# Kernel tuning notes

Hardware: AMD Instinct MI355X
Metric: run time of the kernel (lower is better)

## Reference

```python
import jax, jax.numpy as jnp
import numpy as np

B, N, D, H, DK, DV = 2, 2048, 1024, 16, 64, 64
NEG = -1000000000.0
EPS = 1e-6


def setup_inputs() -> dict:
    key = jax.random.key(0)
    ks = jax.random.split(key, 8)
    s = 0.02
    return {
        "q": jax.random.normal(ks[0], (B, N, D), jnp.float32),
        "k": jax.random.normal(ks[1], (B, N, D), jnp.float32),
        "v": jax.random.normal(ks[2], (B, N, D), jnp.float32),
        "attn_mask": jnp.ones((B, N, N), jnp.int32),
        "Wq": jax.random.normal(ks[3], (D, H * DK), jnp.float32) * s,
        "Wk": jax.random.normal(ks[4], (D, H * DK), jnp.float32) * s,
        "Wv": jax.random.normal(ks[5], (D, H * DV), jnp.float32) * s,
        "Wo": jax.random.normal(ks[6], (H * DV, D), jnp.float32) * s,
        "gamma": jnp.ones((D,), jnp.float32),
        "beta": jnp.zeros((D,), jnp.float32),
    }


def reference(q, k, v, attn_mask, Wq, Wk, Wv, Wo, gamma, beta):
    b, n, _ = q.shape
    residual = q
    # project and split heads: (b, h, n, dk)
    qh = (q @ Wq).reshape(b, n, H, DK).transpose(0, 2, 1, 3)
    kh = (k @ Wk).reshape(b, n, H, DK).transpose(0, 2, 1, 3)
    vh = (v @ Wv).reshape(b, n, H, DV).transpose(0, 2, 1, 3)
    temperature = DK ** 0.5
    scores = jnp.einsum('bhnd,bhmd->bhnm', qh / temperature, kh)
    # external mask (masked where mask == 0), broadcast over heads
    scores = jnp.where(attn_mask[:, None, :, :] == 0, NEG, scores)
    # built-in causal mask (strictly upper triangle)
    causal = jnp.triu(jnp.ones((n, n), dtype=bool), k=1)
    scores = jnp.where(causal, NEG, scores)
    attn = jax.nn.softmax(scores, axis=-1)
    out = jnp.einsum('bhnm,bhmd->bnhd', attn, vh).reshape(b, n, H * DV)
    out = out @ Wo + residual
    # LayerNorm(eps=1e-6)
    mean = out.mean(-1, keepdims=True)
    var = ((out - mean) ** 2).mean(-1, keepdims=True)
    out = (out - mean) / jnp.sqrt(var + EPS) * gamma + beta
    return out, attn
```

## Files before the change

kernel.cpp:

```cpp
#include <hip/hip_runtime.h>
#include <hip/hip_bf16.h>
#include <stdint.h>

#define B_ 2
#define N_ 2048
#define D_ 1024
#define H_ 16
#define MM 4096
#define NN 1024
#define KK 1024

typedef __bf16 bf16;
typedef __bf16 bf16x8 __attribute__((ext_vector_type(8)));
typedef float f32x4 __attribute__((ext_vector_type(4)));

struct __align__(8) bf4 { bf16 v[4]; };

#define LDS_STRIDE 144
#define PSTR 272
#define LOG2E 1.44269504088896340736f

__global__ __launch_bounds__(256) void k_prep(const float* __restrict__ Wq,
                                              const float* __restrict__ Wk,
                                              const float* __restrict__ Wv,
                                              const float* __restrict__ Wo,
                                              const int* __restrict__ mask,
                                              bf16* __restrict__ WqT,
                                              bf16* __restrict__ WkT,
                                              bf16* __restrict__ WvT,
                                              bf16* __restrict__ WoT,
                                              uint32_t* __restrict__ bits) {
    __shared__ float tl[32][33];
    const int bid = blockIdx.x;
    if (bid < 4096) {
        const int z = bid >> 10, t = bid & 1023;
        const float* W = z == 0 ? Wq : z == 1 ? Wk : z == 2 ? Wv : Wo;
        bf16* Wt = z == 0 ? WqT : z == 1 ? WkT : z == 2 ? WvT : WoT;
        const int bx = (t & 31) * 32, by = (t >> 5) * 32;
        const int tx = threadIdx.x & 31, ty = threadIdx.x >> 5;
#pragma unroll
        for (int j = 0; j < 32; j += 8)
            tl[ty + j][tx] = W[(size_t)(by + ty + j) * 1024 + bx + tx];
        __syncthreads();
#pragma unroll
        for (int j = 0; j < 32; j += 8)
            Wt[(size_t)(bx + ty + j) * 1024 + by + tx] = (bf16)tl[tx][ty + j];
    } else {
        size_t flat = (size_t)(bid - 4096) * 256 + threadIdx.x;
        int col = (int)(flat & (N_ - 1));
        int row = (int)((flat >> 11) & (N_ - 1));
        bool ok = (mask[flat] != 0) && (col <= row);
        unsigned long long bal = __ballot(ok);
        if ((threadIdx.x & 63) == 0)
            *(unsigned long long*)(bits + (flat >> 5)) = bal;
    }
}

template <bool AF32>
__device__ __forceinline__ void kb_core(const void* __restrict__ Av,
                                        const bf16* __restrict__ Bt,
                                        int bm0, int bn0,
                                        char* AsB, char* BsB,
                                        f32x4 (&acc)[4][2]) {
    const int tid = threadIdx.x, lane = tid & 63, w = tid >> 6;
    const int g = lane >> 4, li = lane & 15;
    const int srow = tid >> 3, sc = tid & 7;
    const bf16* Ab = (const bf16*)Av;
    const float* Af = (const float*)Av;

    f32x4 zz = {0.f, 0.f, 0.f, 0.f};
#pragma unroll
    for (int mf = 0; mf < 4; ++mf)
#pragma unroll
        for (int nf = 0; nf < 2; ++nf) acc[mf][nf] = zz;

    f32x4 pa0[2], pa1[2];
    bf16x8 pab[2];
    bf16x8 pb[4];

    auto issueA = [&](int k0) {
        if constexpr (AF32) {
#pragma unroll
            for (int i = 0; i < 2; ++i) {
                const float* s = Af + (size_t)(bm0 + srow + 32 * i) * KK + k0 + sc * 8;
                pa0[i] = *(const f32x4*)s;
                pa1[i] = *(const f32x4*)(s + 4);
            }
        } else {
#pragma unroll
            for (int i = 0; i < 2; ++i)
                pab[i] = *(const bf16x8*)(Ab + (size_t)(bm0 + srow + 32 * i) * KK + k0 + sc * 8);
        }
    };
    auto issueB = [&](int k0) {
#pragma unroll
        for (int i = 0; i < 4; ++i)
            pb[i] = *(const bf16x8*)(Bt + (size_t)(bn0 + srow + 32 * i) * KK + k0 + sc * 8);
    };
    auto writeS = [&]() {
#pragma unroll
        for (int i = 0; i < 2; ++i) {
            bf16x8 t;
            if constexpr (AF32) {
#pragma unroll
                for (int j = 0; j < 4; ++j) {
                    t[j] = (bf16)pa0[i][j];
                    t[4 + j] = (bf16)pa1[i][j];
                }
            } else {
                t = pab[i];
            }
            *(bf16x8*)(AsB + (srow + 32 * i) * LDS_STRIDE + sc * 16) = t;
        }
#pragma unroll
        for (int i = 0; i < 4; ++i)
            *(bf16x8*)(BsB + (srow + 32 * i) * LDS_STRIDE + sc * 16) = pb[i];
    };

    issueA(0);
    issueB(0);
    for (int k0 = 0; k0 < KK; k0 += 64) {
        __syncthreads();
        writeS();
        int kn = (k0 + 64 < KK) ? k0 + 64 : k0;
        issueA(kn);
        issueB(kn);
        __syncthreads();
#pragma unroll
        for (int kk = 0; kk < 2; ++kk) {
            const int kb = kk * 64 + (g << 4);
            bf16x8 bfr[2];
#pragma unroll
            for (int nf = 0; nf < 2; ++nf) {
                int rn = w * 32 + nf * 16 + li;
                bfr[nf] = *(const bf16x8*)(BsB + rn * LDS_STRIDE + kb);
            }
#pragma unroll
            for (int mf = 0; mf < 4; ++mf) {
                int rm = mf * 16 + li;
                bf16x8 afr = *(const bf16x8*)(AsB + rm * LDS_STRIDE + kb);
                acc[mf][0] = __builtin_amdgcn_mfma_f32_16x16x32_bf16(
                    afr, bfr[0], acc[mf][0], 0, 0, 0);
                acc[mf][1] = __builtin_amdgcn_mfma_f32_16x16x32_bf16(
                    afr, bfr[1], acc[mf][1], 0, 0, 0);
            }
        }
    }
}

__global__ __launch_bounds__(256) void k_proj3(const float* __restrict__ q,
                                               const float* __restrict__ k,
                                               const float* __restrict__ v,
                                               const bf16* __restrict__ WqT,
                                               const bf16* __restrict__ WkT,
                                               const bf16* __restrict__ WvT,
                                               bf16* __restrict__ Qh,
                                               bf16* __restrict__ Kh,
                                               bf16* __restrict__ Vt) {
    __shared__ __align__(16) char AsB[64 * LDS_STRIDE];
    __shared__ __align__(16) char BsB[128 * LDS_STRIDE];
    const int z = blockIdx.z;
    const float* A = z == 0 ? q : z == 1 ? k : v;
    const bf16* Bt = z == 0 ? WqT : z == 1 ? WkT : WvT;
    const float scale = (z == 0) ? 0.125f * LOG2E : 1.0f;
    const int bm0 = blockIdx.x * 64, bn0 = blockIdx.y * 128;

    f32x4 acc[4][2];
    kb_core<true>(A, Bt, bm0, bn0, AsB, BsB, acc);

    const int tid = threadIdx.x, lane = tid & 63, w = tid >> 6;
    const int g = lane >> 4, li = lane & 15;

    if (z < 2) {
        bf16* C = (z == 0) ? Qh : Kh;
#pragma unroll
        for (int mf = 0; mf < 4; ++mf)
#pragma unroll
            for (int nf = 0; nf < 2; ++nf) {
                int n = bn0 + w * 32 + nf * 16 + li;
                int m0 = bm0 + mf * 16 + (g << 2);
#pragma unroll
                for (int r = 0; r < 4; ++r)
                    C[(size_t)(m0 + r) * NN + n] = (bf16)(acc[mf][nf][r] * scale);
            }
    } else {
#pragma unroll
        for (int mf = 0; mf < 4; ++mf)
#pragma unroll
            for (int nf = 0; nf < 2; ++nf) {
                int n = bn0 + w * 32 + nf * 16 + li;
                int m0 = bm0 + mf * 16 + (g << 2);
                int bq = m0 >> 11, tok = m0 & (N_ - 1);
                int hh = n >> 6, dv = n & 63;
                bf4 val;
#pragma unroll
                for (int r = 0; r < 4; ++r) val.v[r] = (bf16)acc[mf][nf][r];
                *(bf4*)(Vt + ((size_t)((bq * H_ + hh) * 64 + dv)) * N_ + tok) = val;
            }
    }
}

__global__ __launch_bounds__(256) void k_out(const bf16* __restrict__ Ob,
                                             const bf16* __restrict__ WoT,
                                             float* __restrict__ outp,
                                             const float* __restrict__ resid) {
    __shared__ __align__(16) char AsB[64 * LDS_STRIDE];
    __shared__ __align__(16) char BsB[128 * LDS_STRIDE];
    const int bm0 = blockIdx.x * 64, bn0 = blockIdx.y * 128;

    f32x4 acc[4][2];
    kb_core<false>(Ob, WoT, bm0, bn0, AsB, BsB, acc);

    const int tid = threadIdx.x, lane = tid & 63, w = tid >> 6;
    const int g = lane >> 4, li = lane & 15;
#pragma unroll
    for (int mf = 0; mf < 4; ++mf)
#pragma unroll
        for (int nf = 0; nf < 2; ++nf) {
            int n = bn0 + w * 32 + nf * 16 + li;
            int m0 = bm0 + mf * 16 + (g << 2);
#pragma unroll
            for (int r = 0; r < 4; ++r) {
                size_t ix = (size_t)(m0 + r) * NN + n;
                outp[ix] = acc[mf][nf][r] + resid[ix];
            }
        }
}

__global__ __launch_bounds__(256) void k_attn(const bf16* __restrict__ Qh,
                                              const bf16* __restrict__ Kh,
                                              const bf16* __restrict__ Vt,
                                              const uint32_t* __restrict__ bits,
                                              float* __restrict__ attnp,
                                              bf16* __restrict__ Ob) {
    __shared__ __align__(16) char Qs[64 * LDS_STRIDE];
    __shared__ __align__(16) char Ks[128 * LDS_STRIDE];
    __shared__ __align__(16) char Vs[64 * PSTR];
    __shared__ __align__(16) char Ps[64 * PSTR];
    const int tid = threadIdx.x, lane = tid & 63, w = tid >> 6;
    const int g = lane >> 4, li = lane & 15;
    const int p = blockIdx.x, h = blockIdx.y, b = blockIdx.z;
    const int srow = tid >> 3, sc = tid & 7;
    const int myrow = w * 16 + li;

    const size_t kbase = ((size_t)b * N_) * D_ + h * 64;
    const size_t vbase = ((size_t)(b * H_ + h) * 64) * N_;
    f32x4 zz = {0.f, 0.f, 0.f, 0.f};

    bf16x8 kr[4], vr[4];
    auto loadK = [&](int jt) {
#pragma unroll
        for (int i = 0; i < 4; ++i)
            kr[i] = *(const bf16x8*)(Kh + kbase +
                (size_t)(jt * 128 + srow + 32 * i) * D_ + sc * 8);
    };
    auto writeK = [&]() {
#pragma unroll
        for (int i = 0; i < 4; ++i)
            *(bf16x8*)(Ks + (srow + 32 * i) * LDS_STRIDE + sc * 16) = kr[i];
    };
    auto loadV = [&](int jt) {
#pragma unroll
        for (int c = 0; c < 4; ++c) {
            int row = srow + 32 * (c & 1);
            int cc = sc + 8 * (c >> 1);
            vr[c] = *(const bf16x8*)(Vt + vbase + (size_t)row * N_ + jt * 128 + cc * 8);
        }
    };
    auto writeV = [&]() {
#pragma unroll
        for (int c = 0; c < 4; ++c) {
            int row = srow + 32 * (c & 1);
            int cc = sc + 8 * (c >> 1);
            *(bf16x8*)(Vs + row * PSTR + cc * 16) = vr[c];
        }
    };

    for (int half = 0; half < 2; ++half) {
        const int qt = half ? (31 - p) : p;
        const int i0 = qt << 6;
        const int R = (qt + 2) >> 1;
        const size_t abase = (((size_t)b * H_ + h) * N_ + i0) * (size_t)N_;

        __syncthreads();
        {
            const bf16* qsrc = Qh + kbase + (size_t)(i0 + srow) * D_ + sc * 8;
            bf16x8 t0 = *(const bf16x8*)qsrc;
            bf16x8 t1 = *(const bf16x8*)(qsrc + (size_t)32 * D_);
            *(bf16x8*)(Qs + srow * LDS_STRIDE + sc * 16) = t0;
            *(bf16x8*)(Qs + (srow + 32) * LDS_STRIDE + sc * 16) = t1;
        }
        const uint32_t* mrow = bits + (((size_t)b * N_ + i0 + myrow) << 6);

        float m = -1e30f, l = 0.f;
        loadK(0);
        for (int jt = 0; jt < R; ++jt) {
            __syncthreads();
            writeK();
            loadK((jt + 1 < R) ? jt + 1 : jt);
            uint4 mw = *(const uint4*)(mrow + (jt << 2));
            __syncthreads();

            f32x4 s[8];
#pragma unroll
            for (int mf = 0; mf < 8; ++mf) s[mf] = zz;
            __builtin_amdgcn_s_setprio(1);
#pragma unroll
            for (int kk = 0; kk < 2; ++kk) {
                const int kb = kk * 64 + (g << 4);
                bf16x8 qf = *(const bf16x8*)(Qs + myrow * LDS_STRIDE + kb);
#pragma unroll
                for (int mf = 0; mf < 8; ++mf) {
                    bf16x8 kf = *(const bf16x8*)(Ks + (mf * 16 + li) * LDS_STRIDE + kb);
                    s[mf] = __builtin_amdgcn_mfma_f32_16x16x32_bf16(kf, qf, s[mf], 0, 0, 0);
                }
            }
            __builtin_amdgcn_s_setprio(0);
            float tmax = m;
#pragma unroll
            for (int mf = 0; mf < 8; ++mf) {
                uint32_t wsel = (mf < 2) ? mw.x : (mf < 4) ? mw.y : (mf < 6) ? mw.z : mw.w;
#pragma unroll
                for (int r = 0; r < 4; ++r) {
                    int sh = (mf & 1) * 16 + g * 4 + r;
                    float xv = ((wsel >> sh) & 1) ? s[mf][r] : -1e9f;
                    s[mf][r] = xv;
                    tmax = fmaxf(tmax, xv);
                }
            }
            tmax = fmaxf(tmax, __shfl_xor(tmax, 16));
            tmax = fmaxf(tmax, __shfl_xor(tmax, 32));
            float ps = 0.f;
#pragma unroll
            for (int mf = 0; mf < 8; ++mf)
#pragma unroll
                for (int r = 0; r < 4; ++r) ps += exp2f(s[mf][r] - tmax);
            ps += __shfl_xor(ps, 16);
            ps += __shfl_xor(ps, 32);
            l = l * exp2f(m - tmax) + ps;
            m = tmax;
        }
        const float ml = m + __log2f(l);

        f32x4 oacc[4];
#pragma unroll
        for (int nf = 0; nf < 4; ++nf) oacc[nf] = zz;

        loadK(0);
        loadV(0);
        for (int jt = 0; jt < R; ++jt) {
            __syncthreads();
            writeK();
            writeV();
            {
                int jn = (jt + 1 < R) ? jt + 1 : jt;
                loadK(jn);
                loadV(jn);
            }
            uint4 mw = *(const uint4*)(mrow + (jt << 2));
            __syncthreads();

            f32x4 s[8];
#pragma unroll
            for (int mf = 0; mf < 8; ++mf) s[mf] = zz;
            __builtin_amdgcn_s_setprio(1);
#pragma unroll
            for (int kk = 0; kk < 2; ++kk) {
                const int kb = kk * 64 + (g << 4);
                bf16x8 qf = *(const bf16x8*)(Qs + myrow * LDS_STRIDE + kb);
#pragma unroll
                for (int mf = 0; mf < 8; ++mf) {
                    bf16x8 kf = *(const bf16x8*)(Ks + (mf * 16 + li) * LDS_STRIDE + kb);
                    s[mf] = __builtin_amdgcn_mfma_f32_16x16x32_bf16(kf, qf, s[mf], 0, 0, 0);
                }
            }
            __builtin_amdgcn_s_setprio(0);

#pragma unroll
            for (int mf = 0; mf < 8; ++mf) {
                uint32_t wsel = (mf < 2) ? mw.x : (mf < 4) ? mw.y : (mf < 6) ? mw.z : mw.w;
#pragma unroll
                for (int r = 0; r < 4; ++r) {
                    int sh = (mf & 1) * 16 + g * 4 + r;
                    float xv = ((wsel >> sh) & 1) ? s[mf][r] : -1e9f;
                    s[mf][r] = exp2f(xv - ml);
                }
                *(f32x4*)(attnp + abase + (size_t)myrow * N_ + (jt << 7) + mf * 16 + g * 4) = s[mf];
                bf4 pk;
#pragma unroll
                for (int r = 0; r < 4; ++r) pk.v[r] = (bf16)s[mf][r];
                *(bf4*)(Ps + myrow * PSTR + (mf * 16 + g * 4) * 2) = pk;
            }
            __builtin_amdgcn_s_setprio(1);
#pragma unroll
            for (int kk = 0; kk < 4; ++kk) {
                const int kb = kk * 64 + (g << 4);
                bf16x8 pf = *(const bf16x8*)(Ps + myrow * PSTR + kb);
#pragma unroll
                for (int nf = 0; nf < 4; ++nf) {
                    bf16x8 vf = *(const bf16x8*)(Vs + (nf * 16 + li) * PSTR + kb);
                    oacc[nf] = __builtin_amdgcn_mfma_f32_16x16x32_bf16(pf, vf, oacc[nf], 0, 0, 0);
                }
            }
            __builtin_amdgcn_s_setprio(0);
        }
#pragma unroll
        for (int nf = 0; nf < 4; ++nf)
#pragma unroll
            for (int r = 0; r < 4; ++r) {
                int gi = i0 + w * 16 + g * 4 + r;
                Ob[((size_t)(b * N_ + gi)) * D_ + h * 64 + nf * 16 + li] = (bf16)oacc[nf][r];
            }
        int zc0 = R << 7;
        if (zc0 < N_) {
            int r = tid >> 2, tc = tid & 3;
            f32x4 z = zz;
            for (int c = zc0 + tc * 4; c < N_; c += 16)
                *(f32x4*)(attnp + abase + (size_t)r * N_ + c) = z;
        }
    }
}

__global__ __launch_bounds__(256) void k_ln(float* __restrict__ out,
                                            const float* __restrict__ gamma,
                                            const float* __restrict__ beta) {
    const int row = blockIdx.x, t = threadIdx.x, lane = t & 63, w = t >> 6;
    float* p = out + (size_t)row * D_;
    f32x4 x = *(const f32x4*)(p + t * 4);
    float s = x[0] + x[1] + x[2] + x[3];
    float s2 = x[0] * x[0] + x[1] * x[1] + x[2] * x[2] + x[3] * x[3];
#pragma unroll
    for (int o = 1; o < 64; o <<= 1) {
        s += __shfl_xor(s, o);
        s2 += __shfl_xor(s2, o);
    }
    __shared__ float r1[4], r2[4];
    if (lane == 0) { r1[w] = s; r2[w] = s2; }
    __syncthreads();
    s = r1[0] + r1[1] + r1[2] + r1[3];
    s2 = r2[0] + r2[1] + r2[2] + r2[3];
    float mean = s * (1.f / D_);
    float var = s2 * (1.f / D_) - mean * mean;
    float rstd = rsqrtf(var + 1e-6f);
    f32x4 gv = *(const f32x4*)(gamma + t * 4);
    f32x4 bv = *(const f32x4*)(beta + t * 4);
    f32x4 y;
#pragma unroll
    for (int c = 0; c < 4; ++c) y[c] = (x[c] - mean) * rstd * gv[c] + bv[c];
    *(f32x4*)(p + t * 4) = y;
}

extern "C" void kernel_launch(void* const* d_in, const int* in_sizes, int n_in,
                              void* d_out, int out_size, void* d_ws,
                              size_t ws_size, hipStream_t stream) {
    (void)in_sizes; (void)n_in; (void)out_size; (void)ws_size;
    const float* q = (const float*)d_in[0];
    const float* k = (const float*)d_in[1];
    const float* v = (const float*)d_in[2];
    const int* msk = (const int*)d_in[3];
    const float* Wq = (const float*)d_in[4];
    const float* Wk = (const float*)d_in[5];
    const float* Wv = (const float*)d_in[6];
    const float* Wo = (const float*)d_in[7];
    const float* gamma = (const float*)d_in[8];
    const float* beta = (const float*)d_in[9];

    float* outp = (float*)d_out;
    float* attnp = outp + (size_t)B_ * N_ * D_;

    const size_t U = (size_t)B_ * N_ * D_;
    const size_t W1 = (size_t)D_ * D_;
    bf16* ws = (bf16*)d_ws;
    bf16* WqT = ws;  ws += W1;
    bf16* WkT = ws;  ws += W1;
    bf16* WvT = ws;  ws += W1;
    bf16* WoT = ws;  ws += W1;
    bf16* Qh = ws;   ws += U;
    bf16* Kh = ws;   ws += U;
    bf16* Vt = ws;   ws += U;
    bf16* Ob = ws;   ws += U;
    uint32_t* bits = (uint32_t*)ws;

    k_prep<<<4096 + (B_ * N_ * N_ / 256), 256, 0, stream>>>(
        Wq, Wk, Wv, Wo, msk, WqT, WkT, WvT, WoT, bits);

    k_proj3<<<dim3(MM / 64, NN / 128, 3), 256, 0, stream>>>(q, k, v, WqT, WkT, WvT, Qh, Kh, Vt);

    k_attn<<<dim3(16, H_, B_), 256, 0, stream>>>(Qh, Kh, Vt, bits, attnp, Ob);

    k_out<<<dim3(MM / 64, NN / 128), 256, 0, stream>>>(Ob, WoT, outp, q);

    k_ln<<<B_ * N_, 256, 0, stream>>>(outp, gamma, beta);
}
```

Baseline: 259.7 us.

## Split attention into separate row-stats kernel and PV/probability kernel

The first pass of the two-pass attention (computing per-row max and log-sum-exp) moves into its own kernel, k_stats, launched with 32 blocks per head, one per query tile, instead of the paired 16. The second kernel reads the precomputed stats from a workspace buffer and only does the probability write and PV product. This gives the stats pass twice as many independent blocks and lighter register and LDS use, at the cost of an extra launch and a small global round-trip for the stats. The stats grid is not balanced across blocks because each block's work depends on its query tile.

Result: slower. 312.0 us (+20.1%).

```diff
diff --git a/kernel.cpp b/kernel.cpp
--- a/kernel.cpp
+++ b/kernel.cpp
@@ -227,12 +227,102 @@
         }
 }
 
-__global__ __launch_bounds__(256) void k_attn(const bf16* __restrict__ Qh,
-                                              const bf16* __restrict__ Kh,
-                                              const bf16* __restrict__ Vt,
-                                              const uint32_t* __restrict__ bits,
-                                              float* __restrict__ attnp,
-                                              bf16* __restrict__ Ob) {
+__global__ __launch_bounds__(256) void k_stats(const bf16* __restrict__ Qh,
+                                               const bf16* __restrict__ Kh,
+                                               const uint32_t* __restrict__ bits,
+                                               float* __restrict__ mlbuf) {
+    __shared__ __align__(16) char Ks[128 * LDS_STRIDE];
+    const int tid = threadIdx.x, lane = tid & 63, w = tid >> 6;
+    const int g = lane >> 4, li = lane & 15;
+    const int srow = tid >> 3, sc = tid & 7;
+    const int myrow = w * 16 + li;
+
+    const int qt = 31 - blockIdx.x;
+    const int h = blockIdx.y, b = blockIdx.z;
+    const int i0 = qt << 6;
+    const int R = (qt + 2) >> 1;
+
+    const size_t kbase = ((size_t)b * N_) * D_ + h * 64;
+    f32x4 zz = {0.f, 0.f, 0.f, 0.f};
+
+    const bf16* qrow = Qh + kbase + (size_t)(i0 + myrow) * D_;
+    const bf16x8 qf0 = *(const bf16x8*)(qrow + g * 8);
+    const bf16x8 qf1 = *(const bf16x8*)(qrow + 32 + g * 8);
+
+    bf16x8 kr[4];
+    auto loadK = [&](int jt) {
+#pragma unroll
+        for (int i = 0; i < 4; ++i)
+            kr[i] = *(const bf16x8*)(Kh + kbase +
+                (size_t)(jt * 128 + srow + 32 * i) * D_ + sc * 8);
+    };
+    auto writeK = [&]() {
+#pragma unroll
+        for (int i = 0; i < 4; ++i)
+            *(bf16x8*)(Ks + (srow + 32 * i) * LDS_STRIDE + sc * 16) = kr[i];
+    };
+
+    const uint32_t* mrow = bits + (((size_t)b * N_ + i0 + myrow) << 6);
+
+    float m = -1e30f, l = 0.f;
+    loadK(0);
+    for (int jt = 0; jt < R; ++jt) {
+        __syncthreads();
+        writeK();
+        loadK((jt + 1 < R) ? jt + 1 : jt);
+        uint4 mw = *(const uint4*)(mrow + (jt << 2));
+        __syncthreads();
+
+        f32x4 s[8];
+#pragma unroll
+        for (int mf = 0; mf < 8; ++mf) s[mf] = zz;
+        __builtin_amdgcn_s_setprio(1);
+#pragma unroll
+        for (int kk = 0; kk < 2; ++kk) {
+            const int kb = kk * 64 + (g << 4);
+            const bf16x8 qf = kk ? qf1 : qf0;
+#pragma unroll
+            for (int mf = 0; mf < 8; ++mf) {
+                bf16x8 kf = *(const bf16x8*)(Ks + (mf * 16 + li) * LDS_STRIDE + kb);
+                s[mf] = __builtin_amdgcn_mfma_f32_16x16x32_bf16(kf, qf, s[mf], 0, 0, 0);
+            }
+        }
+        __builtin_amdgcn_s_setprio(0);
+        float tmax = m;
+#pragma unroll
+        for (int mf = 0; mf < 8; ++mf) {
+            uint32_t wsel = (mf < 2) ? mw.x : (mf < 4) ? mw.y : (mf < 6) ? mw.z : mw.w;
+#pragma unroll
+            for (int r = 0; r < 4; ++r) {
+                int sh = (mf & 1) * 16 + g * 4 + r;
+                float xv = ((wsel >> sh) & 1) ? s[mf][r] : -1e9f;
+                s[mf][r] = xv;
+                tmax = fmaxf(tmax, xv);
+            }
+        }
+        tmax = fmaxf(tmax, __shfl_xor(tmax, 16));
+        tmax = fmaxf(tmax, __shfl_xor(tmax, 32));
+        float ps = 0.f;
+#pragma unroll
+        for (int mf = 0; mf < 8; ++mf)
+#pragma unroll
+            for (int r = 0; r < 4; ++r) ps += exp2f(s[mf][r] - tmax);
+        ps += __shfl_xor(ps, 16);
+        ps += __shfl_xor(ps, 32);
+        l = l * exp2f(m - tmax) + ps;
+        m = tmax;
+    }
+    if (g == 0)
+        mlbuf[(size_t)(b * H_ + h) * N_ + i0 + myrow] = m + __log2f(l);
+}
+
+__global__ __launch_bounds__(256) void k_pv(const bf16* __restrict__ Qh,
+                                            const bf16* __restrict__ Kh,
+                                            const bf16* __restrict__ Vt,
+                                            const uint32_t* __restrict__ bits,
+                                            const float* __restrict__ mlbuf,
+                                            float* __restrict__ attnp,
+                                            bf16* __restrict__ Ob) {
     __shared__ __align__(16) char Qs[64 * LDS_STRIDE];
     __shared__ __align__(16) char Ks[128 * LDS_STRIDE];
     __shared__ __align__(16) char Vs[64 * PSTR];
@@ -291,56 +381,7 @@
             *(bf16x8*)(Qs + (srow + 32) * LDS_STRIDE + sc * 16) = t1;
         }
         const uint32_t* mrow = bits + (((size_t)b * N_ + i0 + myrow) << 6);
-
-        float m = -1e30f, l = 0.f;
-        loadK(0);
-        for (int jt = 0; jt < R; ++jt) {
-            __syncthreads();
-            writeK();
-            loadK((jt + 1 < R) ? jt + 1 : jt);
-            uint4 mw = *(const uint4*)(mrow + (jt << 2));
-            __syncthreads();
-
-            f32x4 s[8];
-#pragma unroll
-            for (int mf = 0; mf < 8; ++mf) s[mf] = zz;
-            __builtin_amdgcn_s_setprio(1);
-#pragma unroll
-            for (int kk = 0; kk < 2; ++kk) {
-                const int kb = kk * 64 + (g << 4);
-                bf16x8 qf = *(const bf16x8*)(Qs + myrow * LDS_STRIDE + kb);
-#pragma unroll
-                for (int mf = 0; mf < 8; ++mf) {
-                    bf16x8 kf = *(const bf16x8*)(Ks + (mf * 16 + li) * LDS_STRIDE + kb);
-                    s[mf] = __builtin_amdgcn_mfma_f32_16x16x32_bf16(kf, qf, s[mf], 0, 0, 0);
-                }
-            }
-            __builtin_amdgcn_s_setprio(0);
-            float tmax = m;
-#pragma unroll
-            for (int mf = 0; mf < 8; ++mf) {
-                uint32_t wsel = (mf < 2) ? mw.x : (mf < 4) ? mw.y : (mf < 6) ? mw.z : mw.w;
-#pragma unroll
-                for (int r = 0; r < 4; ++r) {
-                    int sh = (mf & 1) * 16 + g * 4 + r;
-                    float xv = ((wsel >> sh) & 1) ? s[mf][r] : -1e9f;
-                    s[mf][r] = xv;
-                    tmax = fmaxf(tmax, xv);
-                }
-            }
-            tmax = fmaxf(tmax, __shfl_xor(tmax, 16));
-            tmax = fmaxf(tmax, __shfl_xor(tmax, 32));
-            float ps = 0.f;
-#pragma unroll
-            for (int mf = 0; mf < 8; ++mf)
-#pragma unroll
-                for (int r = 0; r < 4; ++r) ps += exp2f(s[mf][r] - tmax);
-            ps += __shfl_xor(ps, 16);
-            ps += __shfl_xor(ps, 32);
-            l = l * exp2f(m - tmax) + ps;
-            m = tmax;
-        }
-        const float ml = m + __log2f(l);
+        const float ml = mlbuf[(size_t)(b * H_ + h) * N_ + i0 + myrow];
 
         f32x4 oacc[4];
 #pragma unroll
@@ -480,13 +521,16 @@
     bf16* Vt = ws;   ws += U;
     bf16* Ob = ws;   ws += U;
     uint32_t* bits = (uint32_t*)ws;
+    float* mlbuf = (float*)(bits + (size_t)B_ * N_ * N_ / 32);
 
     k_prep<<<4096 + (B_ * N_ * N_ / 256), 256, 0, stream>>>(
         Wq, Wk, Wv, Wo, msk, WqT, WkT, WvT, WoT, bits);
 
     k_proj3<<<dim3(MM / 64, NN / 128, 3), 256, 0, stream>>>(q, k, v, WqT, WkT, WvT, Qh, Kh, Vt);
 
-    k_attn<<<dim3(16, H_, B_), 256, 0, stream>>>(Qh, Kh, Vt, bits, attnp, Ob);
+    k_stats<<<dim3(32, H_, B_), 256, 0, stream>>>(Qh, Kh, bits, mlbuf);
+
+    k_pv<<<dim3(16, H_, B_), 256, 0, stream>>>(Qh, Kh, Vt, bits, mlbuf, attnp, Ob);
 
     k_out<<<dim3(MM / 64, NN / 128), 256, 0, stream>>>(Ob, WoT, outp, q);
 
```
